# Performance work log

Measured on AMD Instinct MI355X. Metric: run time of the kernel, lower is better.

## Reference

```python
import jax, jax.numpy as jnp
import numpy as np

B, Lq, C = 2, 4096, 768
H, W = 64, 64                 # single feature level, Lin = H*W = 4096
NH, NL, NP = 6, 1, 4          # heads, levels, sampling points
HD = C // NH                  # 128 per-head dim (deform_ratio = 1.0)
EPS = 1e-6
INIT_VALUES = 0.01


def _ln(x, w, b):
    m = jnp.mean(x, axis=-1, keepdims=True)
    xc = x - m
    v = jnp.mean(xc * xc, axis=-1, keepdims=True)
    return xc * jax.lax.rsqrt(v + EPS) * w + b


def _bilinear_gather(v, px, py, h, w):
    # v: [B,NH,h*w,HD]; px,py: [B,NH,Lq,NP] pixel coords (align_corners=False,
    # zero padding) -- matches F.grid_sample used by the pytorch fallback and
    # the Deformable-DETR CUDA kernel.
    x0 = jnp.floor(px); y0 = jnp.floor(py)
    fx = px - x0;       fy = py - y0
    x0i = x0.astype(jnp.int32); y0i = y0.astype(jnp.int32)
    out = 0.
    for dy, dx, wt in ((0, 0, (1 - fy) * (1 - fx)),
                       (0, 1, (1 - fy) * fx),
                       (1, 0, fy * (1 - fx)),
                       (1, 1, fy * fx)):
        yi = y0i + dy; xi = x0i + dx
        valid = ((yi >= 0) & (yi < h) & (xi >= 0) & (xi < w)).astype(v.dtype)
        idx = jnp.clip(yi, 0, h - 1) * w + jnp.clip(xi, 0, w - 1)  # [B,NH,Lq,NP]
        g = jnp.take_along_axis(v, idx.reshape(idx.shape[0], idx.shape[1], -1, 1), axis=2)
        g = g.reshape(idx.shape + (v.shape[-1],))                  # [B,NH,Lq,NP,HD]
        out = out + g * (wt * valid)[..., None]
    return out


def _ms_deform_attn_core(value, sampling_locations, attention_weights):
    # value [B,H*W,NH,HD]; locations [B,Lq,NH,NL,NP,2] in [0,1]; weights [B,Lq,NH,NL,NP]
    v = value.transpose(0, 2, 1, 3)                                 # [B,NH,HW,HD]
    loc = sampling_locations[:, :, :, 0].transpose(0, 2, 1, 3, 4)   # level 0: [B,NH,Lq,NP,2]
    px = loc[..., 0] * W - 0.5
    py = loc[..., 1] * H - 0.5
    sampled = _bilinear_gather(v, px, py, H, W)                     # [B,NH,Lq,NP,HD]
    aw = attention_weights[:, :, :, 0].transpose(0, 2, 1, 3)        # [B,NH,Lq,NP]
    out = jnp.einsum('bhqpd,bhqp->bqhd', sampled, aw)
    return out.reshape(B, Lq, NH * HD)


def setup_inputs() -> dict:
    key = jax.random.key(0)
    k = jax.random.split(key, 8)
    s = 0.02
    return {
        'x': jax.random.normal(k[0], (B, Lq, C), jnp.float32),
        'reference_points': jax.random.uniform(k[1], (B, Lq, NL, 2), jnp.float32),
        'feat': jax.random.normal(k[2], (B, H * W, C), jnp.float32),
        'spatial_shapes': jnp.array([[H, W]], jnp.int32),
        'level_start_index': jnp.zeros((1,), jnp.int32),
        'qn_w': jnp.ones((C,), jnp.float32),
        'qn_b': jnp.zeros((C,), jnp.float32),
        'fn_w': jnp.ones((C,), jnp.float32),
        'fn_b': jnp.zeros((C,), jnp.float32),
        'gamma': jnp.full((C,), INIT_VALUES, jnp.float32),
        'w_value': jax.random.normal(k[3], (C, C), jnp.float32) * s,
        'b_value': jnp.zeros((C,), jnp.float32),
        'w_off': jax.random.normal(k[4], (C, NH * NL * NP * 2), jnp.float32) * s,
        'b_off': jax.random.uniform(k[5], (NH * NL * NP * 2,), jnp.float32, -2.0, 2.0),
        'w_attn': jax.random.normal(k[6], (C, NH * NL * NP), jnp.float32) * s,
        'b_attn': jnp.zeros((NH * NL * NP,), jnp.float32),
        'w_out': jax.random.normal(k[7], (C, C), jnp.float32) * s,
        'b_out': jnp.zeros((C,), jnp.float32),
    }


def reference(x, reference_points, feat, spatial_shapes, level_start_index,
              qn_w, qn_b, fn_w, fn_b, gamma,
              w_value, b_value, w_off, b_off, w_attn, b_attn, w_out, b_out):
    q = _ln(x, qn_w, qn_b)
    f = _ln(feat, fn_w, fn_b)
    value = (f @ w_value + b_value).reshape(B, H * W, NH, HD)
    off = (q @ w_off + b_off).reshape(B, Lq, NH, NL, NP, 2)
    aw = (q @ w_attn + b_attn).reshape(B, Lq, NH, NL * NP)
    aw = jax.nn.softmax(aw, axis=-1).reshape(B, Lq, NH, NL, NP)
    # offset_normalizer = (W_l, H_l) per level
    norm = jnp.array([W, H], dtype=x.dtype)
    loc = reference_points[:, :, None, :, None, :] + off / norm    # [B,Lq,NH,NL,NP,2]
    attn = _ms_deform_attn_core(value, loc, aw)
    attn = attn @ w_out + b_out
    return x + gamma * attn
```

## Files before the change

### kernel.cpp

```cpp
#include <hip/hip_runtime.h>
#include <cstdint>
#include <cstddef>

typedef unsigned short u16;
typedef unsigned int u32;
typedef __bf16 bf16x8 __attribute__((ext_vector_type(8)));
typedef float f32x4 __attribute__((ext_vector_type(4)));

static constexpr int CDIM = 768;
static constexpr int NROWS = 8192;
static constexpr int ASTR = 72;

__device__ __forceinline__ u16 f2bf(float f) {
  union { float f; u32 u; } v; v.f = f;
  return (u16)((v.u + 0x7fffu + ((v.u >> 16) & 1u)) >> 16);
}
__device__ __forceinline__ float bf2f(u16 h) {
  union { u32 u; float f; } v; v.u = ((u32)h) << 16;
  return v.f;
}
__device__ __forceinline__ float ldf(const void* p, size_t i, int F) {
  return F ? ((const float*)p)[i] : bf2f(((const u16*)p)[i]);
}

__global__ __launch_bounds__(256) void detect_kernel(const u16* __restrict__ x, int* __restrict__ flag) {
  int t = threadIdx.x;
  int cnt = 0;
  for (int i = t; i < 16384; i += 256) {
    u16 v = x[i];
    if ((v & 0x7F80u) == 0x7F80u) cnt++;
  }
  #pragma unroll
  for (int m = 32; m >= 1; m >>= 1) cnt += __shfl_xor(cnt, m, 64);
  __shared__ int r[4];
  if ((t & 63) == 0) r[t >> 6] = cnt;
  __syncthreads();
  if (t == 0) flag[0] = (r[0] + r[1] + r[2] + r[3] > 4) ? 1 : 0;
}

__global__ __launch_bounds__(192) void ln_kernel(
    const void* __restrict__ x, const void* __restrict__ feat,
    const void* __restrict__ qw, const void* __restrict__ qb,
    const void* __restrict__ fw, const void* __restrict__ fb,
    u16* __restrict__ qout, u16* __restrict__ fout, const int* __restrict__ flagp) {
  const int F = *flagp;
  int row = blockIdx.x;
  const void *src, *w, *b; u16* dst; size_t base;
  if (row < NROWS) { src = x; base = (size_t)row*CDIM; w = qw; b = qb; dst = qout + base; }
  else { int r2 = row - NROWS; src = feat; base = (size_t)r2*CDIM; w = fw; b = fb; dst = fout + (size_t)r2*CDIM; }
  int t = threadIdx.x;
  float v[4];
  if (F) {
    float4 q = ((const float4*)((const float*)src + base))[t];
    v[0]=q.x; v[1]=q.y; v[2]=q.z; v[3]=q.w;
  } else {
    const u16* sp = (const u16*)src + base + t*4;
    v[0]=bf2f(sp[0]); v[1]=bf2f(sp[1]); v[2]=bf2f(sp[2]); v[3]=bf2f(sp[3]);
  }
  float s = v[0]+v[1]+v[2]+v[3];
  float sq = v[0]*v[0]+v[1]*v[1]+v[2]*v[2]+v[3]*v[3];
  #pragma unroll
  for (int m = 32; m >= 1; m >>= 1) { s += __shfl_xor(s, m, 64); sq += __shfl_xor(sq, m, 64); }
  __shared__ float red[6];
  int lane = t & 63, wv = t >> 6;
  if (lane == 0) { red[wv] = s; red[wv+3] = sq; }
  __syncthreads();
  s  = red[0]+red[1]+red[2];
  sq = red[3]+red[4]+red[5];
  float mean = s * (1.f/768.f);
  float var  = fmaxf(sq * (1.f/768.f) - mean*mean, 0.f);
  float inv  = rsqrtf(var + 1e-6f);
  u16 o[4];
  #pragma unroll
  for (int k = 0; k < 4; ++k) {
    float wk = ldf(w, t*4+k, F), bk = ldf(b, t*4+k, F);
    o[k] = f2bf((v[k]-mean)*inv*wk + bk);
  }
  *(ushort4*)(dst + t*4) = make_ushort4(o[0], o[1], o[2], o[3]);
}

__global__ __launch_bounds__(256) void transpose_wt(
    const void* __restrict__ wv_, const void* __restrict__ wo_,
    u16* __restrict__ wvT, u16* __restrict__ woT, const int* __restrict__ flagp) {
  const int F = *flagp;
  __shared__ u16 tile[32][33];
  const void* in = blockIdx.z ? wo_ : wv_;
  u16* out       = blockIdx.z ? woT : wvT;
  int bn = blockIdx.x * 32;
  int bk = blockIdx.y * 32;
  int tx = threadIdx.x & 31, ty = threadIdx.x >> 5;
  #pragma unroll
  for (int i = ty; i < 32; i += 8)
    tile[i][tx] = F ? f2bf(((const float*)in)[(size_t)(bk+i)*CDIM + bn + tx])
                    : ((const u16*)in)[(size_t)(bk+i)*CDIM + bn + tx];
  __syncthreads();
  #pragma unroll
  for (int i = ty; i < 32; i += 8)
    out[(size_t)(bn+i)*CDIM + bk + tx] = tile[tx][i];
}

__global__ __launch_bounds__(256) void build_woffaw(
    const void* __restrict__ woff, const void* __restrict__ wattn, u16* __restrict__ outT,
    const int* __restrict__ flagp) {
  const int F = *flagp;
  int idx = blockIdx.x * 256 + threadIdx.x;
  if (idx >= 128 * CDIM) return;
  int n = idx / CDIM, k = idx - n*CDIM;
  float v = 0.f;
  if (n < 48)      v = ldf(woff, (size_t)k*48 + n, F);
  else if (n < 72) v = ldf(wattn, (size_t)k*24 + (n-48), F);
  outT[idx] = f2bf(v);
}

template<int EPI>
__global__ __launch_bounds__(256) void gemm_bt(
    const u16* __restrict__ A, const u16* __restrict__ Bt, void* __restrict__ Cout,
    const void* __restrict__ bias0, const void* __restrict__ bias1,
    const void* __restrict__ xres, const void* __restrict__ gammap,
    const int* __restrict__ flagp) {
  const int F = *flagp;
  __shared__ __align__(16) u16 smem[(128+64)*ASTR];
  u16* As = smem;
  u16* Bs = smem + 128*ASTR;
  u16* Cs = smem;
  const int m0 = blockIdx.x * 128;
  const int n0 = blockIdx.y * 64;
  const int t = threadIdx.x, lane = t & 63, wv = t >> 6;
  const int wm = wv & 1, wn = wv >> 1;
  const int kChunk = CDIM / gridDim.z;
  const int kbase = blockIdx.z * kChunk;
  const int lr = lane >> 3;
  const int lc = (lane & 7) * 8;
  f32x4 acc[4][2] = {};

  for (int kk = 0; kk < kChunk; kk += 64) {
    const int k0 = kbase + kk;
    #pragma unroll
    for (int j = 0; j < 4; ++j) {
      int row = (wv*4 + j)*8 + lr;
      *(bf16x8*)(As + row*ASTR + lc) = *(const bf16x8*)(A + (size_t)(m0+row)*CDIM + k0 + lc);
    }
    #pragma unroll
    for (int j = 0; j < 2; ++j) {
      int row = (wv*2 + j)*8 + lr;
      *(bf16x8*)(Bs + row*ASTR + lc) = *(const bf16x8*)(Bt + (size_t)(n0+row)*CDIM + k0 + lc);
    }
    __syncthreads();
    #pragma unroll
    for (int u = 0; u < 2; ++u) {
      bf16x8 af[4], bfr[2];
      const int kc = u*32 + (lane >> 4)*8;
      #pragma unroll
      for (int i = 0; i < 4; ++i)
        af[i]  = *(const bf16x8*)(As + (wm*64 + i*16 + (lane & 15))*ASTR + kc);
      #pragma unroll
      for (int j = 0; j < 2; ++j)
        bfr[j] = *(const bf16x8*)(Bs + (wn*32 + j*16 + (lane & 15))*ASTR + kc);
      #pragma unroll
      for (int i = 0; i < 4; ++i)
        #pragma unroll
        for (int j = 0; j < 2; ++j)
          acc[i][j] = __builtin_amdgcn_mfma_f32_16x16x32_bf16(af[i], bfr[j], acc[i][j], 0, 0, 0);
    }
    __syncthreads();
  }

  const int r0 = (lane >> 4) * 4;
  const int c  = lane & 15;

  if (EPI == 1) {
    float* op = (float*)Cout + (size_t)blockIdx.z * NROWS * 72;
    #pragma unroll
    for (int i = 0; i < 4; ++i)
      #pragma unroll
      for (int j = 0; j < 2; ++j) {
        int col = n0 + wn*32 + j*16 + c;
        if (col < 72) {
          float bb = 0.f;
          if (blockIdx.z == 0) bb = (col < 48) ? ldf(bias0, col, F) : ldf(bias1, col-48, F);
          #pragma unroll
          for (int r = 0; r < 4; ++r)
            op[(size_t)(m0 + wm*64 + i*16 + r0 + r)*72 + col] = acc[i][j][r] + bb;
        }
      }
    return;
  }

  #pragma unroll
  for (int i = 0; i < 4; ++i)
    #pragma unroll
    for (int j = 0; j < 2; ++j) {
      int col = wn*32 + j*16 + c;
      float bb = ldf(bias0, n0 + col, F);
      #pragma unroll
      for (int r = 0; r < 4; ++r)
        Cs[(wm*64 + i*16 + r0 + r)*64 + col] = f2bf(acc[i][j][r] + bb);
    }
  __syncthreads();
  #pragma unroll
  for (int it = 0; it < 4; ++it) {
    int idx = it*256 + t;
    int row = idx >> 3, colb = (idx & 7) * 8;
    size_t gbase = (size_t)(m0 + row)*CDIM + n0 + colb;
    const u16* cp = Cs + row*64 + colb;
    if (EPI == 0) {
      *(bf16x8*)((u16*)Cout + gbase) = *(const bf16x8*)cp;
    } else {
      if (F) {
        const float* xp = (const float*)xres + gbase;
        const float* gp = (const float*)gammap + n0 + colb;
        float4 x0 = *(const float4*)xp,      x1 = *(const float4*)(xp + 4);
        float4 g0 = *(const float4*)gp,      g1 = *(const float4*)(gp + 4);
        float4 o0, o1;
        o0.x = x0.x + g0.x*bf2f(cp[0]); o0.y = x0.y + g0.y*bf2f(cp[1]);
        o0.z = x0.z + g0.z*bf2f(cp[2]); o0.w = x0.w + g0.w*bf2f(cp[3]);
        o1.x = x1.x + g1.x*bf2f(cp[4]); o1.y = x1.y + g1.y*bf2f(cp[5]);
        o1.z = x1.z + g1.z*bf2f(cp[6]); o1.w = x1.w + g1.w*bf2f(cp[7]);
        *(float4*)((float*)Cout + gbase)     = o0;
        *(float4*)((float*)Cout + gbase + 4) = o1;
      } else {
        const u16* xp = (const u16*)xres + gbase;
        const u16* gp = (const u16*)gammap + n0 + colb;
        u16 ov[8];
        #pragma unroll
        for (int k = 0; k < 8; ++k)
          ov[k] = f2bf(bf2f(xp[k]) + bf2f(gp[k]) * bf2f(cp[k]));
        *(bf16x8*)((u16*)Cout + gbase) = *(const bf16x8*)ov;
      }
    }
  }
}

__global__ __launch_bounds__(256) void sample_kernel(
    const u16* __restrict__ value,
    const float* __restrict__ offawp,
    const void* __restrict__ refp,
    u16* __restrict__ out, const int* __restrict__ flagp) {
  const int F = *flagp;
  const int wq   = blockIdx.x * 4 + (threadIdx.x >> 6);
  const int lane = threadIdx.x & 63;
  const int row  = wq / 3;
  const int h0   = (wq % 3) * 2;
  const int b    = row >> 12;
  const float* p0 = offawp + (size_t)row*72;
  const float* p1 = p0 + (size_t)NROWS*72;
  float rx = ldf(refp, (size_t)row*2,   F) * 64.f - 0.5f;
  float ry = ldf(refp, (size_t)row*2+1, F) * 64.f - 0.5f;

  float wts[2][16]; int offs[2][16];
  #pragma unroll
  for (int s = 0; s < 2; ++s) {
    const int h = h0 + s;
    float ob[8], aw4[4];
    #pragma unroll
    for (int k = 0; k < 8; ++k) ob[k] = p0[h*8+k] + p1[h*8+k];
    #pragma unroll
    for (int k = 0; k < 4; ++k) aw4[k] = p0[48+h*4+k] + p1[48+h*4+k];
    float mx = fmaxf(fmaxf(aw4[0],aw4[1]), fmaxf(aw4[2],aw4[3]));
    float e0 = __expf(aw4[0]-mx), e1 = __expf(aw4[1]-mx), e2 = __expf(aw4[2]-mx), e3 = __expf(aw4[3]-mx);
    float rs = 1.f / (e0+e1+e2+e3);
    float awt[4] = {e0*rs, e1*rs, e2*rs, e3*rs};
    #pragma unroll
    for (int p = 0; p < 4; ++p) {
      float px = rx + ob[p*2];
      float py = ry + ob[p*2+1];
      float x0f = floorf(px), y0f = floorf(py);
      float fx = px - x0f, fy = py - y0f;
      int x0 = (int)x0f, y0 = (int)y0f;
      #pragma unroll
      for (int dy = 0; dy < 2; ++dy)
        #pragma unroll
        for (int dx = 0; dx < 2; ++dx) {
          int yi = y0 + dy, xi = x0 + dx;
          bool valid = (yi >= 0) & (yi < 64) & (xi >= 0) & (xi < 64);
          float wt = (dy ? fy : 1.f-fy) * (dx ? fx : 1.f-fx) * awt[p];
          wts[s][p*4+dy*2+dx] = valid ? wt : 0.f;
          int yc = min(max(yi, 0), 63), xc = min(max(xi, 0), 63);
          offs[s][p*4+dy*2+dx] = (yc*64 + xc) * 384;
        }
    }
  }
  const u32* vbase = (const u32*)value + (size_t)b*4096*384 + h0*64 + lane;
  u32 vals[2][16];
  #pragma unroll
  for (int s = 0; s < 2; ++s)
    #pragma unroll
    for (int i = 0; i < 16; ++i)
      vals[s][i] = (vbase + s*64)[offs[s][i]];
  #pragma unroll
  for (int s = 0; s < 2; ++s) {
    float accx = 0.f, accy = 0.f;
    #pragma unroll
    for (int i = 0; i < 16; ++i) {
      accx += wts[s][i] * bf2f((u16)(vals[s][i] & 0xffffu));
      accy += wts[s][i] * bf2f((u16)(vals[s][i] >> 16));
    }
    ((u32*)out)[(size_t)row*384 + (h0+s)*64 + lane] = (u32)f2bf(accx) | ((u32)f2bf(accy) << 16);
  }
}

extern "C" void kernel_launch(void* const* d_in, const int* in_sizes, int n_in,
                              void* d_out, int out_size, void* d_ws, size_t ws_size,
                              hipStream_t stream) {
  const void* x       = d_in[0];
  const void* refp    = d_in[1];
  const void* feat    = d_in[2];
  const void* qn_w    = d_in[5];
  const void* qn_b    = d_in[6];
  const void* fn_w    = d_in[7];
  const void* fn_b    = d_in[8];
  const void* gamma   = d_in[9];
  const void* w_value = d_in[10];
  const void* b_value = d_in[11];
  const void* w_off   = d_in[12];
  const void* b_off   = d_in[13];
  const void* w_attn  = d_in[14];
  const void* b_attn  = d_in[15];
  const void* w_out   = d_in[16];
  const void* b_out   = d_in[17];

  char* p = (char*)d_ws;
  const size_t act = (size_t)NROWS * CDIM * 2;
  u16* q_bf   = (u16*)p; p += act;
  u16* f_bf   = (u16*)p; p += act;
  u16* val_bf = (u16*)p; p += act;
  u16* wvT    = (u16*)p; p += (size_t)CDIM*CDIM*2;
  u16* woT    = (u16*)p; p += (size_t)CDIM*CDIM*2;
  u16* woaT   = (u16*)p; p += (size_t)128*CDIM*2;
  float* offawp = (float*)p; p += (size_t)2*NROWS*72*4;
  int* dflag  = (int*)p; p += 256;
  u16* samp_bf = q_bf;

  detect_kernel<<<dim3(1), 256, 0, stream>>>((const u16*)x, dflag);
  transpose_wt<<<dim3(24,24,2), 256, 0, stream>>>(w_value, w_out, wvT, woT, dflag);
  build_woffaw<<<dim3(384), 256, 0, stream>>>(w_off, w_attn, woaT, dflag);
  ln_kernel<<<dim3(16384), 192, 0, stream>>>(x, feat, qn_w, qn_b, fn_w, fn_b, q_bf, f_bf, dflag);
  gemm_bt<0><<<dim3(64,12,1), 256, 0, stream>>>(f_bf, wvT, val_bf, b_value, nullptr, nullptr, nullptr, dflag);
  gemm_bt<1><<<dim3(64,2,2),  256, 0, stream>>>(q_bf, woaT, offawp, b_off, b_attn, nullptr, nullptr, dflag);
  sample_kernel<<<dim3(6144), 256, 0, stream>>>(val_bf, offawp, refp, samp_bf, dflag);
  gemm_bt<2><<<dim3(64,12,1), 256, 0, stream>>>(samp_bf, woT, d_out, b_out, nullptr, x, gamma, dflag);
}
```

Measured before the change: 241.3 us.

## Use direct global-to-LDS loads in GEMM, merge weight prep, raise split-K

The GEMM tile loads now use the global_load_lds builtin to copy 16-byte chunks straight into shared memory, with a k-split layout of 32-wide panels instead of a padded row stride. This removes the register round trip on staging. The offset/attention GEMM moves from split-K 2 to 4 and the sampler sums four partials. The two weight preparation kernels are merged into one launch. The unpadded 32-element row stride may cause LDS bank conflicts on the fragment reads.

```diff
diff --git a/kernel.cpp b/kernel.cpp
--- a/kernel.cpp
+++ b/kernel.cpp
@@ -1,6 +1,9 @@
 #include <hip/hip_runtime.h>
 #include <cstdint>
 #include <cstddef>
+
+#define GLOBAL_AS __attribute__((address_space(1)))
+#define LDS_AS __attribute__((address_space(3)))
 
 typedef unsigned short u16;
 typedef unsigned int u32;
@@ -9,7 +12,7 @@
 
 static constexpr int CDIM = 768;
 static constexpr int NROWS = 8192;
-static constexpr int ASTR = 72;
+static constexpr int KS1 = 4;
 
 __device__ __forceinline__ u16 f2bf(float f) {
   union { float f; u32 u; } v; v.f = f;
@@ -21,6 +24,9 @@
 }
 __device__ __forceinline__ float ldf(const void* p, size_t i, int F) {
   return F ? ((const float*)p)[i] : bf2f(((const u16*)p)[i]);
+}
+__device__ __forceinline__ void load_lds16(const u16* g, u16* l) {
+  __builtin_amdgcn_global_load_lds((const GLOBAL_AS u32*)g, (LDS_AS u32*)l, 16, 0, 0);
 }
 
 __global__ __launch_bounds__(256) void detect_kernel(const u16* __restrict__ x, int* __restrict__ flag) {
@@ -79,10 +85,22 @@
   *(ushort4*)(dst + t*4) = make_ushort4(o[0], o[1], o[2], o[3]);
 }
 
-__global__ __launch_bounds__(256) void transpose_wt(
+__global__ __launch_bounds__(256) void prep_kernel(
     const void* __restrict__ wv_, const void* __restrict__ wo_,
-    u16* __restrict__ wvT, u16* __restrict__ woT, const int* __restrict__ flagp) {
+    const void* __restrict__ woff, const void* __restrict__ wattn,
+    u16* __restrict__ wvT, u16* __restrict__ woT, u16* __restrict__ woaT,
+    const int* __restrict__ flagp) {
   const int F = *flagp;
+  if (blockIdx.z == 2) {
+    int idx = (blockIdx.y * 24 + blockIdx.x) * 256 + threadIdx.x;
+    if (idx >= 128 * CDIM) return;
+    int n = idx / CDIM, k = idx - n*CDIM;
+    float v = 0.f;
+    if (n < 48)      v = ldf(woff, (size_t)k*48 + n, F);
+    else if (n < 72) v = ldf(wattn, (size_t)k*24 + (n-48), F);
+    woaT[idx] = f2bf(v);
+    return;
+  }
   __shared__ u16 tile[32][33];
   const void* in = blockIdx.z ? wo_ : wv_;
   u16* out       = blockIdx.z ? woT : wvT;
@@ -97,19 +115,6 @@
   #pragma unroll
   for (int i = ty; i < 32; i += 8)
     out[(size_t)(bn+i)*CDIM + bk + tx] = tile[tx][i];
-}
-
-__global__ __launch_bounds__(256) void build_woffaw(
-    const void* __restrict__ woff, const void* __restrict__ wattn, u16* __restrict__ outT,
-    const int* __restrict__ flagp) {
-  const int F = *flagp;
-  int idx = blockIdx.x * 256 + threadIdx.x;
-  if (idx >= 128 * CDIM) return;
-  int n = idx / CDIM, k = idx - n*CDIM;
-  float v = 0.f;
-  if (n < 48)      v = ldf(woff, (size_t)k*48 + n, F);
-  else if (n < 72) v = ldf(wattn, (size_t)k*24 + (n-48), F);
-  outT[idx] = f2bf(v);
 }
 
 template<int EPI>
@@ -119,9 +124,9 @@
     const void* __restrict__ xres, const void* __restrict__ gammap,
     const int* __restrict__ flagp) {
   const int F = *flagp;
-  __shared__ __align__(16) u16 smem[(128+64)*ASTR];
+  __shared__ __align__(16) u16 smem[12288];
   u16* As = smem;
-  u16* Bs = smem + 128*ASTR;
+  u16* Bs = smem + 8192;
   u16* Cs = smem;
   const int m0 = blockIdx.x * 128;
   const int n0 = blockIdx.y * 64;
@@ -129,33 +134,36 @@
   const int wm = wv & 1, wn = wv >> 1;
   const int kChunk = CDIM / gridDim.z;
   const int kbase = blockIdx.z * kChunk;
-  const int lr = lane >> 3;
-  const int lc = (lane & 7) * 8;
+  const int lrow = lane >> 2;
+  const int lcol = (lane & 3) * 8;
   f32x4 acc[4][2] = {};
 
-  for (int kk = 0; kk < kChunk; kk += 64) {
-    const int k0 = kbase + kk;
+  for (int k0 = kbase; k0 < kbase + kChunk; k0 += 64) {
     #pragma unroll
     for (int j = 0; j < 4; ++j) {
-      int row = (wv*4 + j)*8 + lr;
-      *(bf16x8*)(As + row*ASTR + lc) = *(const bf16x8*)(A + (size_t)(m0+row)*CDIM + k0 + lc);
+      int g = wv*4 + j;
+      int p = g >> 3, s = g & 7;
+      load_lds16(A + (size_t)(m0 + s*16 + lrow)*CDIM + k0 + p*32 + lcol,
+                 As + p*4096 + s*512);
     }
     #pragma unroll
     for (int j = 0; j < 2; ++j) {
-      int row = (wv*2 + j)*8 + lr;
-      *(bf16x8*)(Bs + row*ASTR + lc) = *(const bf16x8*)(Bt + (size_t)(n0+row)*CDIM + k0 + lc);
+      int g = wv*2 + j;
+      int p = g >> 2, s = g & 3;
+      load_lds16(Bt + (size_t)(n0 + s*16 + lrow)*CDIM + k0 + p*32 + lcol,
+                 Bs + p*2048 + s*512);
     }
     __syncthreads();
     #pragma unroll
     for (int u = 0; u < 2; ++u) {
       bf16x8 af[4], bfr[2];
-      const int kc = u*32 + (lane >> 4)*8;
+      const int kc = (lane >> 4) * 8;
       #pragma unroll
       for (int i = 0; i < 4; ++i)
-        af[i]  = *(const bf16x8*)(As + (wm*64 + i*16 + (lane & 15))*ASTR + kc);
+        af[i]  = *(const bf16x8*)(As + u*4096 + (wm*64 + i*16 + (lane & 15))*32 + kc);
       #pragma unroll
       for (int j = 0; j < 2; ++j)
-        bfr[j] = *(const bf16x8*)(Bs + (wn*32 + j*16 + (lane & 15))*ASTR + kc);
+        bfr[j] = *(const bf16x8*)(Bs + u*2048 + (wn*32 + j*16 + (lane & 15))*32 + kc);
       #pragma unroll
       for (int i = 0; i < 4; ++i)
         #pragma unroll
@@ -242,8 +250,7 @@
   const int row  = wq / 3;
   const int h0   = (wq % 3) * 2;
   const int b    = row >> 12;
-  const float* p0 = offawp + (size_t)row*72;
-  const float* p1 = p0 + (size_t)NROWS*72;
+  const float* pr = offawp + (size_t)row*72;
   float rx = ldf(refp, (size_t)row*2,   F) * 64.f - 0.5f;
   float ry = ldf(refp, (size_t)row*2+1, F) * 64.f - 0.5f;
 
@@ -253,9 +260,19 @@
     const int h = h0 + s;
     float ob[8], aw4[4];
     #pragma unroll
-    for (int k = 0; k < 8; ++k) ob[k] = p0[h*8+k] + p1[h*8+k];
-    #pragma unroll
-    for (int k = 0; k < 4; ++k) aw4[k] = p0[48+h*4+k] + p1[48+h*4+k];
+    for (int k = 0; k < 8; ++k) {
+      float v = 0.f;
+      #pragma unroll
+      for (int z = 0; z < KS1; ++z) v += pr[(size_t)z*NROWS*72 + h*8 + k];
+      ob[k] = v;
+    }
+    #pragma unroll
+    for (int k = 0; k < 4; ++k) {
+      float v = 0.f;
+      #pragma unroll
+      for (int z = 0; z < KS1; ++z) v += pr[(size_t)z*NROWS*72 + 48 + h*4 + k];
+      aw4[k] = v;
+    }
     float mx = fmaxf(fmaxf(aw4[0],aw4[1]), fmaxf(aw4[2],aw4[3]));
     float e0 = __expf(aw4[0]-mx), e1 = __expf(aw4[1]-mx), e2 = __expf(aw4[2]-mx), e3 = __expf(aw4[3]-mx);
     float rs = 1.f / (e0+e1+e2+e3);
@@ -327,16 +344,15 @@
   u16* wvT    = (u16*)p; p += (size_t)CDIM*CDIM*2;
   u16* woT    = (u16*)p; p += (size_t)CDIM*CDIM*2;
   u16* woaT   = (u16*)p; p += (size_t)128*CDIM*2;
-  float* offawp = (float*)p; p += (size_t)2*NROWS*72*4;
+  float* offawp = (float*)p; p += (size_t)KS1*NROWS*72*4;
   int* dflag  = (int*)p; p += 256;
   u16* samp_bf = q_bf;
 
   detect_kernel<<<dim3(1), 256, 0, stream>>>((const u16*)x, dflag);
-  transpose_wt<<<dim3(24,24,2), 256, 0, stream>>>(w_value, w_out, wvT, woT, dflag);
-  build_woffaw<<<dim3(384), 256, 0, stream>>>(w_off, w_attn, woaT, dflag);
+  prep_kernel<<<dim3(24,24,3), 256, 0, stream>>>(w_value, w_out, w_off, w_attn, wvT, woT, woaT, dflag);
   ln_kernel<<<dim3(16384), 192, 0, stream>>>(x, feat, qn_w, qn_b, fn_w, fn_b, q_bf, f_bf, dflag);
-  gemm_bt<0><<<dim3(64,12,1), 256, 0, stream>>>(f_bf, wvT, val_bf, b_value, nullptr, nullptr, nullptr, dflag);
-  gemm_bt<1><<<dim3(64,2,2),  256, 0, stream>>>(q_bf, woaT, offawp, b_off, b_attn, nullptr, nullptr, dflag);
+  gemm_bt<0><<<dim3(64,12,1),   256, 0, stream>>>(f_bf, wvT, val_bf, b_value, nullptr, nullptr, nullptr, dflag);
+  gemm_bt<1><<<dim3(64,2,KS1),  256, 0, stream>>>(q_bf, woaT, offawp, b_off, b_attn, nullptr, nullptr, dflag);
   sample_kernel<<<dim3(6144), 256, 0, stream>>>(val_bf, offawp, refp, samp_bf, dflag);
-  gemm_bt<2><<<dim3(64,12,1), 256, 0, stream>>>(samp_bf, woT, d_out, b_out, nullptr, x, gamma, dflag);
-}
+  gemm_bt<2><<<dim3(64,12,1),   256, 0, stream>>>(samp_bf, woT, d_out, b_out, nullptr, x, gamma, dflag);
+}
```

Measured after the change: 232.8 us. 3.5% less time.
